# Kernel optimization log

Measured on AMD Instinct MI355X. Metric: run time of the kernel, lower is better.

Reference implementation:

```python
import jax, jax.numpy as jnp
import numpy as np

R = 6            # search radius
P = 2 * R + 1    # patch size = 13
D = 4            # mask downsample rate
TOPK = 36        # top-k over patch dim (eval path)


def _corr(fq, fm):
    """Local correlation volume (SpatialCorrelationSampler, kernel=1, patch=P).
    fq, fm: [b,c,h,w] -> [b, P*P, h*w]."""
    b, c, h, w = fq.shape
    fmp = jnp.pad(fm, ((0, 0), (0, 0), (R, R), (R, R)))
    rows = []
    for di in range(P):
        for dj in range(P):
            rows.append(jnp.einsum('bchw,bchw->bhw', fq, fmp[:, :, di:di + h, dj:dj + w]))
    return jnp.stack(rows, 1).reshape(b, P * P, h * w)


def _unfold(msk):
    """F.unfold(msk, kernel_size=P, padding=R): [b,o,h,w] -> [b,o,P*P,h*w]."""
    b, o, h, w = msk.shape
    mp = jnp.pad(msk, ((0, 0), (0, 0), (R, R), (R, R)))
    pats = [mp[:, :, di:di + h, dj:dj + w] for di in range(P) for dj in range(P)]
    return jnp.stack(pats, 2).reshape(b, o, P * P, h * w)


def _forward(feat_query, feat_mem0, feat_mem1, msk_mem0, msk_mem1):
    b, c, h, w = feat_query.shape
    # correlation volumes for each memory frame, concat over patch dim
    corr = jnp.concatenate([_corr(feat_query, feat_mem0),
                            _corr(feat_query, feat_mem1)], axis=1)
    corr = corr / jnp.sqrt(jnp.asarray(c, corr.dtype))          # [b, 2*P*P, N]
    # eval path: top-k over the (frames*P*P) patch axis, per pixel
    corr_t = corr.transpose(0, 2, 1)                              # [b, N, 2PP]
    vals, idx = jax.lax.top_k(corr_t, TOPK)                       # [b, N, K]
    wts = jax.nn.softmax(vals, axis=-1)                           # [b, N, K]
    # downsample masks by strided slicing, unfold, concat over patch dim
    msk = jnp.concatenate([_unfold(msk_mem0[:, :, ::D, ::D]),
                           _unfold(msk_mem1[:, :, ::D, ::D])], axis=2)  # [b,o,2PP,N]
    msk_t = msk.transpose(0, 3, 1, 2)                             # [b, N, o, 2PP]
    g = jnp.take_along_axis(msk_t, idx[:, :, None, :], axis=3)    # [b, N, o, K]
    out = (wts[:, :, None, :] * g).sum(-1)                        # [b, N, o]
    obj = msk_mem0.shape[1]
    return out.transpose(0, 2, 1).reshape(b, obj, h, w)


def setup_inputs() -> dict:
    key = jax.random.key(0)
    k = jax.random.split(key, 5)
    b, c, h, w = 1, 256, 120, 216
    obj = 11
    return {
        'feat_query': jax.random.normal(k[0], (b, c, h, w), jnp.float32),
        'feat_mem0': jax.random.normal(k[1], (b, c, h, w), jnp.float32),
        'feat_mem1': jax.random.normal(k[2], (b, c, h, w), jnp.float32),
        'msk_mem0': jax.random.uniform(k[3], (b, obj, h * D, w * D), jnp.float32),
        'msk_mem1': jax.random.uniform(k[4], (b, obj, h * D, w * D), jnp.float32),
    }


def reference(feat_query, feat_mem0, feat_mem1, msk_mem0, msk_mem1):
    return _forward(feat_query, feat_mem0, feat_mem1, msk_mem0, msk_mem1)
```

## Files before the change

kernel.cpp:

```cpp
#include <hip/hip_runtime.h>
#include <hip/hip_bf16.h>
#include <math.h>

#define H 120
#define W 216
#define C 256
#define NPIX (H*W)
#define PATCH 13
#define PP 169
#define RAD 6
#define TOPKN 36
#define OBJ 11
#define MD 4
#define CW 344

typedef unsigned short ushort;
typedef unsigned int   uint;
typedef __attribute__((ext_vector_type(8))) __bf16 bf16x8;
typedef __attribute__((ext_vector_type(4))) float   f32x4;

#define PLANE_B ((size_t)NPIX * 512)

#define YT 8
#define RT 20
#define XT 16
#define UW 32
#define PXS 128
#define ROWS (UW * PXS)
#define NXT 14
#define NYT 15
#define NWG (NXT * 2 * NYT)

__device__ inline ushort f2bf_rne(float x) {
  uint u = __float_as_uint(x);
  uint r = (u + 0x7FFFu + ((u >> 16) & 1u)) >> 16;
  return (ushort)r;
}
__device__ inline float bf2f(ushort h) { return __uint_as_float(((uint)h) << 16); }

__global__ __launch_bounds__(256) void k_prep(const float* __restrict__ fq,
                      const float* __restrict__ fm0, const float* __restrict__ fm1,
                      char* fqt, char* fm0t, char* fm1t) {
  const float* src = (blockIdx.z == 0) ? fq : (blockIdx.z == 1) ? fm0 : fm1;
  char* dst = (blockIdx.z == 0) ? fqt : (blockIdx.z == 1) ? fm0t : fm1t;

  const int p0 = blockIdx.x * 64;
  const int c0 = blockIdx.y * 64;
  const int tid = threadIdx.x;

  __shared__ float ts[64 * 65];
  {
    int p = tid & 63, cl = tid >> 6;
    #pragma unroll
    for (int jj = 0; jj < 16; ++jj) {
      int c = 4 * jj + cl;
      ts[c * 65 + p] = src[(size_t)(c0 + c) * NPIX + p0 + p];
    }
  }
  __syncthreads();
  {
    int pl = tid >> 2, sub = tid & 3;
    ushort hb[16], lb[16];
    #pragma unroll
    for (int i = 0; i < 16; ++i) {
      float x = ts[(sub * 16 + i) * 65 + pl];
      ushort h = f2bf_rne(x);
      hb[i] = h;
      lb[i] = f2bf_rne(x - bf2f(h));
    }
    size_t off = (size_t)(p0 + pl) * 512 + (size_t)c0 * 2 + sub * 32;
    *(uint4*)(dst + off)            = ((uint4*)hb)[0];
    *(uint4*)(dst + off + 16)       = ((uint4*)hb)[1];
    *(uint4*)(dst + PLANE_B + off)      = ((uint4*)lb)[0];
    *(uint4*)(dst + PLANE_B + off + 16) = ((uint4*)lb)[1];
  }
}

__global__ void k_downsample(const float* __restrict__ m0, const float* __restrict__ m1,
                             float* __restrict__ mds) {
  int i = blockIdx.x * 256 + threadIdx.x;
  const int total = 2 * OBJ * NPIX;
  if (i >= total) return;
  int fo = i / NPIX;
  int pix = i - fo * NPIX;
  int f = fo / OBJ, o = fo - f * OBJ;
  int y = pix / W, x = pix - y * W;
  const float* src = f ? m1 : m0;
  mds[i] = src[(size_t)o * (H*MD) * (W*MD) + (size_t)(MD*y) * (W*MD) + MD*x];
}

__global__ __launch_bounds__(512, 2) void k_corr_mfma(const char* __restrict__ fqt,
                        const char* __restrict__ fm0t, const char* __restrict__ fm1t,
                        float* __restrict__ corr) {
  int b = blockIdx.x;
  int xcd = b & 7;
  int wgid = ((xcd < 4) ? xcd * 53 : 4 * 53 + (xcd - 4) * 52) + (b >> 3);
  int yt   = wgid % NYT;
  int rest = wgid / NYT;
  int f    = rest & 1;
  int xt   = rest >> 1;

  const int y0 = yt * YT;
  const int X0 = xt * XT;
  const int tid  = threadIdx.x;
  const int wy   = tid >> 6;
  const int lane = tid & 63;
  const int l15  = lane & 15, l4 = lane >> 4;
  const int y    = y0 + wy;

  const char* frame = f ? fm1t : fm0t;

  __shared__ __align__(16) char bsm[RT * ROWS];

  uint soff[10], ldso[10];
  #pragma unroll
  for (int s = 0; s < 10; ++s) {
    int g  = tid + 512 * s;
    int ri = g >> 8;
    int rem = g & 255;
    int px = rem >> 3;
    int p  = (rem >> 2) & 1;
    int q  = rem & 3;
    int r  = y0 - 6 + ri;  r = (r < 0) ? 0 : (r >= H ? H - 1 : r);
    int u  = X0 - 8 + px;  u = (u < 0) ? 0 : (u >= W ? W - 1 : u);
    ldso[s] = (uint)((ri * ROWS + px * PXS + p * 64 + q * 16) ^ ((px & 7) << 4));
    soff[s] = (uint)(p * PLANE_B + (size_t)(r * W + u) * 512 + q * 16);
  }

  int xA = X0 + l15;
  const char* pa = fqt + (size_t)(y * W + (xA < W ? xA : W - 1)) * 512 + l4 * 16;
  bf16x8 Ah[8], Al[8];
  #pragma unroll
  for (int kc = 0; kc < 8; ++kc) {
    Ah[kc] = *(const bf16x8*)(pa + kc * 64);
    Al[kc] = *(const bf16x8*)(pa + PLANE_B + kc * 64);
  }

  const int px0 = l15, px1 = 16 + l15;
  const uint sw  = (uint)((l15 & 7) << 4);
  const uint b0h = (uint)((px0 * PXS +      l4 * 16) ^ sw);
  const uint b0l = (uint)((px0 * PXS + 64 + l4 * 16) ^ sw);
  const uint b1h = (uint)((px1 * PXS +      l4 * 16) ^ sw);
  const uint b1l = (uint)((px1 * PXS + 64 + l4 * 16) ^ sw);

  int u0 = X0 + l15 - 8;
  int u1 = u0 + 16;
  bool uok0 = (u0 >= 0) && (u0 < W);
  bool uok1 = (u1 >= 0) && (u1 < W);

  f32x4 acc[13][2];
  #pragma unroll
  for (int di = 0; di < 13; ++di) {
    acc[di][0] = (f32x4){0.f, 0.f, 0.f, 0.f};
    acc[di][1] = (f32x4){0.f, 0.f, 0.f, 0.f};
  }

  for (int kc = 0; kc < 8; ++kc) {
    #pragma unroll
    for (int s = 0; s < 10; ++s)
      *(uint4*)(bsm + ldso[s]) = *(const uint4*)(frame + (size_t)soff[s] + kc * 64);
    __syncthreads();

    #pragma unroll
    for (int di = 0; di < 13; ++di) {
      int rr = y + di - RAD;
      if (rr >= 0 && rr < H) {
        const char* rb = bsm + (wy + di) * ROWS;
        {
          bf16x8 Bhv = *(const bf16x8*)(rb + b0h);
          bf16x8 Blv = *(const bf16x8*)(rb + b0l);
          acc[di][0] = __builtin_amdgcn_mfma_f32_16x16x32_bf16(Ah[kc], Bhv, acc[di][0], 0, 0, 0);
          acc[di][0] = __builtin_amdgcn_mfma_f32_16x16x32_bf16(Ah[kc], Blv, acc[di][0], 0, 0, 0);
          acc[di][0] = __builtin_amdgcn_mfma_f32_16x16x32_bf16(Al[kc], Bhv, acc[di][0], 0, 0, 0);
        }
        {
          bf16x8 Bhv = *(const bf16x8*)(rb + b1h);
          bf16x8 Blv = *(const bf16x8*)(rb + b1l);
          acc[di][1] = __builtin_amdgcn_mfma_f32_16x16x32_bf16(Ah[kc], Bhv, acc[di][1], 0, 0, 0);
          acc[di][1] = __builtin_amdgcn_mfma_f32_16x16x32_bf16(Ah[kc], Blv, acc[di][1], 0, 0, 0);
          acc[di][1] = __builtin_amdgcn_mfma_f32_16x16x32_bf16(Al[kc], Bhv, acc[di][1], 0, 0, 0);
        }
      }
    }
    __syncthreads();
  }

  float* cb = corr + (size_t)(y * W) * CW + f * PP;
  #pragma unroll
  for (int di = 0; di < 13; ++di) {
    #pragma unroll
    for (int nt = 0; nt < 2; ++nt) {
      bool uok = nt ? uok1 : uok0;
      #pragma unroll
      for (int j = 0; j < 4; ++j) {
        int m  = l4 * 4 + j;
        int x  = X0 + m;
        int dj = 16 * nt + l15 - m - 2;
        if (x < W && dj >= 0 && dj < PATCH)
          cb[(size_t)x * CW + di * PATCH + dj] = uok ? acc[di][nt][j] * 0.0625f : 0.f;
      }
    }
  }
}

__global__ __launch_bounds__(64) void k_corr_valu(const float* __restrict__ fq,
                       const float* __restrict__ fm0, const float* __restrict__ fm1,
                       float* __restrict__ corr) {
  int b = blockIdx.x;
  int lb = (b & 7) * 390 + (b >> 3);
  int y   = lb / 26;
  int r26 = lb - y * 26;
  int f   = r26 / 13;
  int di  = r26 - f * 13;
  const int tid = threadIdx.x;
  const int xg  = tid;
  const int r   = y + di - RAD;

  float* corr_base = corr + (size_t)(y * W) * CW + (f * PP + di * PATCH);

  if (r < 0 || r >= H) {
    if (xg < 54) {
      float* cp = corr_base + (size_t)(4 * xg) * CW;
      #pragma unroll
      for (int sub = 0; sub < 4; ++sub) {
        #pragma unroll
        for (int dj = 0; dj < PATCH; ++dj) cp[(size_t)sub * CW + dj] = 0.f;
      }
    }
    return;
  }

  const float* fm = f ? fm1 : fm0;
  __shared__ float fm_s[4 * 232];

  const float* pf[4];
  int  ldsoff[4];
  bool sval[4], mval[4];
  #pragma unroll
  for (int s = 0; s < 4; ++s) {
    int i = tid + 64 * s;
    sval[s] = (i < 232);
    int ii = sval[s] ? i : 0;
    int ch = ii / 58;
    int m  = ii - ch * 58;
    int x  = 4 * m - 8;
    mval[s] = sval[s] && (m >= 2) && (m <= 55);
    ldsoff[s] = ch * 232 + 4 * m;
    pf[s] = fm + (size_t)ch * NPIX + (size_t)r * W + (mval[s] ? x : 0);
  }

  const float* pq = fq + (size_t)y * W + 4 * ((xg < 54) ? xg : 0);

  float4 acc[PATCH];
  #pragma unroll
  for (int d = 0; d < PATCH; ++d) acc[d] = make_float4(0.f, 0.f, 0.f, 0.f);

  for (int c0 = 0; c0 < C; c0 += 4) {
    #pragma unroll
    for (int s = 0; s < 4; ++s) {
      if (sval[s]) {
        float4 v = make_float4(0.f, 0.f, 0.f, 0.f);
        if (mval[s]) v = *(const float4*)(pf[s]);
        *(float4*)&fm_s[ldsoff[s]] = v;
        pf[s] += 4 * (size_t)NPIX;
      }
    }
    __syncthreads();
    if (xg < 54) {
      #pragma unroll
      for (int ch = 0; ch < 4; ++ch) {
        float4 q4 = *(const float4*)(pq + (size_t)ch * NPIX);
        float rv[20];
        #pragma unroll
        for (int qq = 0; qq < 5; ++qq) {
          float4 t4 = *(const float4*)&fm_s[ch * 232 + 4 * xg + 4 * qq];
          rv[4*qq+0] = t4.x; rv[4*qq+1] = t4.y; rv[4*qq+2] = t4.z; rv[4*qq+3] = t4.w;
        }
        #pragma unroll
        for (int dj = 0; dj < PATCH; ++dj) {
          acc[dj].x += q4.x * rv[dj + 2];
          acc[dj].y += q4.y * rv[dj + 3];
          acc[dj].z += q4.z * rv[dj + 4];
          acc[dj].w += q4.w * rv[dj + 5];
        }
      }
      pq += 4 * (size_t)NPIX;
    }
    __syncthreads();
  }

  if (xg < 54) {
    float* cp = corr_base + (size_t)(4 * xg) * CW;
    #pragma unroll
    for (int dj = 0; dj < PATCH; ++dj) {
      cp[dj]                  = acc[dj].x * 0.0625f;
      cp[(size_t)1 * CW + dj] = acc[dj].y * 0.0625f;
      cp[(size_t)2 * CW + dj] = acc[dj].z * 0.0625f;
      cp[(size_t)3 * CW + dj] = acc[dj].w * 0.0625f;
    }
  }
}

__global__ __launch_bounds__(256) void k_topk(const float* __restrict__ corr,
                       const float* __restrict__ mds, float* __restrict__ out) {
  int wid = (blockIdx.x * 256 + threadIdx.x) >> 6;
  int lane = threadIdx.x & 63;
  if (wid >= NPIX) return;
  const float* cr = corr + (size_t)wid * CW;

  float v[6]; uint ui[6];
  #pragma unroll
  for (int s = 0; s < 6; ++s) {
    int idx = lane + 64 * s;
    bool ok = idx < 2 * PP;
    float f = ok ? cr[idx] : 0.f;
    v[s] = f;
    uint bb = __float_as_uint(f);
    uint u = bb ^ (uint)(((int)bb >> 31) | 0x80000000);
    ui[s] = ok ? u : 0u;
  }

  uint blo = 0u, bhi = 0xFFFFFFFFu;
  for (int it = 0; it < 32; ++it) {
    uint mid = blo + ((bhi - blo) >> 1);
    int c = 0;
    #pragma unroll
    for (int s = 0; s < 6; ++s)
      c += __popcll(__ballot(ui[s] > mid));
    if (c <= 35) bhi = mid; else blo = mid + 1;
  }
  const uint x0 = blo;

  int c_gt = 0;
  #pragma unroll
  for (int s = 0; s < 6; ++s) c_gt += __popcll(__ballot(ui[s] > x0));
  const int need = 36 - c_gt;

  uint tb = (x0 & 0x80000000u) ? (x0 ^ 0x80000000u) : ~x0;
  const float tf = __uint_as_float(tb);

  float w[6];
  float zp = 0.f;
  int prior = 0;
  #pragma unroll
  for (int s = 0; s < 6; ++s) {
    unsigned long long tie = __ballot(ui[s] == x0);
    uint below = __builtin_amdgcn_mbcnt_hi((uint)(tie >> 32),
                  __builtin_amdgcn_mbcnt_lo((uint)tie, 0u));
    bool acc = (ui[s] > x0) || ((ui[s] == x0) && ((prior + (int)below) < need));
    prior += __popcll(tie);
    w[s] = acc ? __expf(v[s] - tf) : 0.f;
    zp += w[s];
  }
  float Z = zp;
  #pragma unroll
  for (int off = 32; off >= 1; off >>= 1) Z += __shfl_xor(Z, off, 64);

  int y = wid / W, x = wid - (wid / W) * W;
  float no[OBJ];
  #pragma unroll
  for (int o = 0; o < OBJ; ++o) no[o] = 0.f;
  #pragma unroll
  for (int s = 0; s < 6; ++s) {
    if (w[s] > 0.f) {
      int idx = lane + 64 * s;
      int ff = idx >= PP;
      int r = idx - ff * PP;
      int di = r / PATCH, dj = r - (r / PATCH) * PATCH;
      int yy = y + di - RAD, xx = x + dj - RAD;
      if (yy >= 0 && yy < H && xx >= 0 && xx < W) {
        const float* mb = mds + ((size_t)ff * OBJ) * NPIX + yy * W + xx;
        #pragma unroll
        for (int o = 0; o < OBJ; ++o) no[o] += w[s] * mb[(size_t)o * NPIX];
      }
    }
  }
  float inv = 1.f / Z;
  #pragma unroll
  for (int o = 0; o < OBJ; ++o) {
    float p = no[o];
    #pragma unroll
    for (int off = 32; off >= 1; off >>= 1) p += __shfl_xor(p, off, 64);
    if (lane == 0) out[(size_t)o * NPIX + wid] = p * inv;
  }
}

extern "C" void kernel_launch(void* const* d_in, const int* in_sizes, int n_in,
                              void* d_out, int out_size, void* d_ws, size_t ws_size,
                              hipStream_t stream) {
  const float* fq  = (const float*)d_in[0];
  const float* fm0 = (const float*)d_in[1];
  const float* fm1 = (const float*)d_in[2];
  const float* m0  = (const float*)d_in[3];
  const float* m1  = (const float*)d_in[4];
  float* out = (float*)d_out;

  char* ws = (char*)d_ws;
  size_t off = 0;
  auto alloc = [&](size_t sz) { size_t o = off; off = (off + sz + 1023) & ~(size_t)1023; return o; };

  size_t mds_o  = alloc((size_t)2 * OBJ * NPIX * sizeof(float));
  size_t corr_o = alloc((size_t)NPIX * CW * sizeof(float));
  size_t fqt_o  = alloc(2 * PLANE_B);
  size_t fm0t_o = alloc(2 * PLANE_B);
  size_t fm1t_o = alloc(2 * PLANE_B);
  size_t needed = off;

  float* mds  = (float*)(ws + mds_o);
  float* corr = (float*)(ws + corr_o);

  k_downsample<<<(2 * OBJ * NPIX + 255) / 256, 256, 0, stream>>>(m0, m1, mds);

  if (ws_size >= needed) {
    char* fqt  = ws + fqt_o;
    char* fm0t = ws + fm0t_o;
    char* fm1t = ws + fm1t_o;
    dim3 gp(405, 4, 3);
    k_prep<<<gp, 256, 0, stream>>>(fq, fm0, fm1, fqt, fm0t, fm1t);
    k_corr_mfma<<<NWG, 512, 0, stream>>>(fqt, fm0t, fm1t, corr);
  } else {
    k_corr_valu<<<120 * 26, 64, 0, stream>>>(fq, fm0, fm1, corr);
  }

  k_topk<<<NPIX / 4, 256, 0, stream>>>(corr, mds, out);
}
```

Before: 141.9 us.

## Register-prefetch next K-chunk of frame tile and query fragments during MFMA compute

The correlation kernel now loads the next channel chunk of the memory-frame tile into registers while MFMAs run on the current chunk, then stores it to shared memory after a barrier. The query A fragments are streamed one chunk at a time instead of preloading all 16 vectors, which lowers register pressure. The barrier moves to the top of each iteration. The aim is to hide global load latency behind matrix compute, at the cost of 10 extra uint4 staging registers per thread.

```diff
diff --git a/kernel.cpp b/kernel.cpp
--- a/kernel.cpp
+++ b/kernel.cpp
@@ -129,12 +129,6 @@
 
   int xA = X0 + l15;
   const char* pa = fqt + (size_t)(y * W + (xA < W ? xA : W - 1)) * 512 + l4 * 16;
-  bf16x8 Ah[8], Al[8];
-  #pragma unroll
-  for (int kc = 0; kc < 8; ++kc) {
-    Ah[kc] = *(const bf16x8*)(pa + kc * 64);
-    Al[kc] = *(const bf16x8*)(pa + PLANE_B + kc * 64);
-  }
 
   const int px0 = l15, px1 = 16 + l15;
   const uint sw  = (uint)((l15 & 7) << 4);
@@ -155,11 +149,32 @@
     acc[di][1] = (f32x4){0.f, 0.f, 0.f, 0.f};
   }
 
+  uint4 pb[10];
+  #pragma unroll
+  for (int s = 0; s < 10; ++s)
+    pb[s] = *(const uint4*)(frame + (size_t)soff[s]);
+  uint4 aC0 = *(const uint4*)(pa);
+  uint4 aC1 = *(const uint4*)(pa + PLANE_B);
+  uint4 aN0, aN1;
+
+  #pragma unroll
   for (int kc = 0; kc < 8; ++kc) {
+    __syncthreads();
     #pragma unroll
     for (int s = 0; s < 10; ++s)
-      *(uint4*)(bsm + ldso[s]) = *(const uint4*)(frame + (size_t)soff[s] + kc * 64);
+      *(uint4*)(bsm + ldso[s]) = pb[s];
     __syncthreads();
+
+    if (kc < 7) {
+      #pragma unroll
+      for (int s = 0; s < 10; ++s)
+        pb[s] = *(const uint4*)(frame + (size_t)soff[s] + (kc + 1) * 64);
+      aN0 = *(const uint4*)(pa + (kc + 1) * 64);
+      aN1 = *(const uint4*)(pa + PLANE_B + (kc + 1) * 64);
+    }
+
+    bf16x8 Ahv = __builtin_bit_cast(bf16x8, aC0);
+    bf16x8 Alv = __builtin_bit_cast(bf16x8, aC1);
 
     #pragma unroll
     for (int di = 0; di < 13; ++di) {
@@ -169,20 +184,20 @@
         {
           bf16x8 Bhv = *(const bf16x8*)(rb + b0h);
           bf16x8 Blv = *(const bf16x8*)(rb + b0l);
-          acc[di][0] = __builtin_amdgcn_mfma_f32_16x16x32_bf16(Ah[kc], Bhv, acc[di][0], 0, 0, 0);
-          acc[di][0] = __builtin_amdgcn_mfma_f32_16x16x32_bf16(Ah[kc], Blv, acc[di][0], 0, 0, 0);
-          acc[di][0] = __builtin_amdgcn_mfma_f32_16x16x32_bf16(Al[kc], Bhv, acc[di][0], 0, 0, 0);
+          acc[di][0] = __builtin_amdgcn_mfma_f32_16x16x32_bf16(Ahv, Bhv, acc[di][0], 0, 0, 0);
+          acc[di][0] = __builtin_amdgcn_mfma_f32_16x16x32_bf16(Ahv, Blv, acc[di][0], 0, 0, 0);
+          acc[di][0] = __builtin_amdgcn_mfma_f32_16x16x32_bf16(Alv, Bhv, acc[di][0], 0, 0, 0);
         }
         {
           bf16x8 Bhv = *(const bf16x8*)(rb + b1h);
           bf16x8 Blv = *(const bf16x8*)(rb + b1l);
-          acc[di][1] = __builtin_amdgcn_mfma_f32_16x16x32_bf16(Ah[kc], Bhv, acc[di][1], 0, 0, 0);
-          acc[di][1] = __builtin_amdgcn_mfma_f32_16x16x32_bf16(Ah[kc], Blv, acc[di][1], 0, 0, 0);
-          acc[di][1] = __builtin_amdgcn_mfma_f32_16x16x32_bf16(Al[kc], Bhv, acc[di][1], 0, 0, 0);
+          acc[di][1] = __builtin_amdgcn_mfma_f32_16x16x32_bf16(Ahv, Bhv, acc[di][1], 0, 0, 0);
+          acc[di][1] = __builtin_amdgcn_mfma_f32_16x16x32_bf16(Ahv, Blv, acc[di][1], 0, 0, 0);
+          acc[di][1] = __builtin_amdgcn_mfma_f32_16x16x32_bf16(Alv, Bhv, acc[di][1], 0, 0, 0);
         }
       }
     }
-    __syncthreads();
+    aC0 = aN0; aC1 = aN1;
   }
 
   float* cb = corr + (size_t)(y * W) * CW + f * PP;
```

Result: slower. 222.8 us (+57.0%).

## Double-buffer correlation LDS tiles with direct global-to-LDS async loads

Applied to the files above, without the earlier changes.

Replaces the register-staged global→LDS copy of the memory-frame tile with global_load_lds direct transfers into a double-buffered LDS region. The next channel chunk is prefetched while MFMAs run on the current one, hiding load latency behind compute. Source addresses are rearranged so the XOR swizzle is applied on the global side, because each lane's LDS destination is now fixed. LDS use doubles, which may reduce occupancy, and the visible part does not show how the synchronisation for the async loads is handled.

```diff
diff --git a/kernel.cpp b/kernel.cpp
--- a/kernel.cpp
+++ b/kernel.cpp
@@ -27,6 +27,7 @@
 #define UW 32
 #define PXS 128
 #define ROWS (UW * PXS)
+#define BUFB (RT * ROWS)
 #define NXT 14
 #define NYT 15
 #define NWG (NXT * 2 * NYT)
@@ -110,21 +111,21 @@
 
   const char* frame = f ? fm1t : fm0t;
 
-  __shared__ __align__(16) char bsm[RT * ROWS];
-
-  uint soff[10], ldso[10];
-  #pragma unroll
-  for (int s = 0; s < 10; ++s) {
-    int g  = tid + 512 * s;
-    int ri = g >> 8;
-    int rem = g & 255;
-    int px = rem >> 3;
-    int p  = (rem >> 2) & 1;
-    int q  = rem & 3;
-    int r  = y0 - 6 + ri;  r = (r < 0) ? 0 : (r >= H ? H - 1 : r);
-    int u  = X0 - 8 + px;  u = (u < 0) ? 0 : (u >= W ? W - 1 : u);
-    ldso[s] = (uint)((ri * ROWS + px * PXS + p * 64 + q * 16) ^ ((px & 7) << 4));
-    soff[s] = (uint)(p * PLANE_B + (size_t)(r * W + u) * 512 + q * 16);
+  __shared__ __align__(16) char bsm[2 * BUFB];
+
+  const char* gsrc[10];
+  #pragma unroll
+  for (int i = 0; i < 10; ++i) {
+    int gdest = wy * 640 + i * 64 + lane;
+    int ri  = gdest >> 8;
+    int rem = gdest & 255;
+    int px  = rem >> 3;
+    int pqp = rem & 7;
+    int pqs = pqp ^ (px & 7);
+    int p   = pqs >> 2, q = pqs & 3;
+    int r = y0 - 6 + ri;  r = (r < 0) ? 0 : (r >= H ? H - 1 : r);
+    int u = X0 - 8 + px;  u = (u < 0) ? 0 : (u >= W ? W - 1 : u);
+    gsrc[i] = frame + (size_t)p * PLANE_B + (size_t)(r * W + u) * 512 + q * 16;
   }
 
   int xA = X0 + l15;
@@ -155,17 +156,28 @@
     acc[di][1] = (f32x4){0.f, 0.f, 0.f, 0.f};
   }
 
+  auto STAGE = [&](int buf, int kc) {
+    #pragma unroll
+    for (int i = 0; i < 10; ++i)
+      __builtin_amdgcn_global_load_lds(
+        (const __attribute__((address_space(1))) void*)(gsrc[i] + kc * 64),
+        (__attribute__((address_space(3))) void*)(bsm + buf * BUFB + wy * 10240 + i * 1024),
+        16, 0, 0);
+  };
+
+  STAGE(0, 0);
+  __syncthreads();
+
+  #pragma unroll
   for (int kc = 0; kc < 8; ++kc) {
-    #pragma unroll
-    for (int s = 0; s < 10; ++s)
-      *(uint4*)(bsm + ldso[s]) = *(const uint4*)(frame + (size_t)soff[s] + kc * 64);
-    __syncthreads();
+    if (kc < 7) STAGE((kc + 1) & 1, kc + 1);
+    const char* bb = bsm + (kc & 1) * BUFB;
 
     #pragma unroll
     for (int di = 0; di < 13; ++di) {
       int rr = y + di - RAD;
       if (rr >= 0 && rr < H) {
-        const char* rb = bsm + (wy + di) * ROWS;
+        const char* rb = bb + (wy + di) * ROWS;
         {
           bf16x8 Bhv = *(const bf16x8*)(rb + b0h);
           bf16x8 Blv = *(const bf16x8*)(rb + b0l);
```

New measurement: 138.5 us. 2.3% less time.
